# Kernel optimization log

Hardware: AMD Instinct MI355X
Metric: run time of the kernel (lower is better)

## Reference

```python
import jax, jax.numpy as jnp
import numpy as np

E, IN, H, OUT = 8, 512, 1024, 512   # num_experts, input_size, hidden_size, output_size
HH = H // 2                          # expert-MLP hidden (512)
GIN, GH = 5, E                       # gating GRU input / hidden


def gru_layer(x, w_ih, w_hh, b_ih, b_hh):
    """torch.nn.GRU single layer, batch_first. x: [B,T,I] -> ys: [B,T,Hd].
    Gate order in 3*Hd dims: reset, update, new."""
    Hd = w_hh.shape[1]
    def step(h, xt):
        gi = xt @ w_ih.T + b_ih          # [B,3Hd]
        gh = h @ w_hh.T + b_hh
        ir, iz, inn = jnp.split(gi, 3, axis=-1)
        hr, hz, hn = jnp.split(gh, 3, axis=-1)
        r = jax.nn.sigmoid(ir + hr)
        z = jax.nn.sigmoid(iz + hz)
        n = jnp.tanh(inn + r * hn)
        h = (1.0 - z) * n + z * h
        return h, h
    h0 = jnp.zeros((x.shape[0], Hd), x.dtype)
    _, ys = jax.lax.scan(step, h0, jnp.swapaxes(x, 0, 1))
    return jnp.swapaxes(ys, 0, 1)


def _uniform(key, shape, fan_in, fan_out):
    bound = np.sqrt(6.0 / (fan_in * fan_out))
    return jax.random.uniform(key, shape, jnp.float32, -bound, bound)


def setup_inputs() -> dict:
    key = jax.random.key(0)
    ks = jax.random.split(key, 16)
    g = 1.0 / np.sqrt(GH)
    m = 1.0 / np.sqrt(H)
    inp = {
        "X": jax.random.normal(ks[0], (128, 100, IN), jnp.float32),
        # gating GRU: 2 layers, input 5 -> hidden E
        "gw_ih0": jax.random.uniform(ks[1], (3 * GH, GIN), jnp.float32, -g, g),
        "gw_hh0": jax.random.uniform(ks[2], (3 * GH, GH), jnp.float32, -g, g),
        "gb_ih0": jnp.zeros((3 * GH,), jnp.float32),
        "gb_hh0": jnp.zeros((3 * GH,), jnp.float32),
        "gw_ih1": jax.random.uniform(ks[3], (3 * GH, GH), jnp.float32, -g, g),
        "gw_hh1": jax.random.uniform(ks[4], (3 * GH, GH), jnp.float32, -g, g),
        "gb_ih1": jnp.zeros((3 * GH,), jnp.float32),
        "gb_hh1": jnp.zeros((3 * GH,), jnp.float32),
        # main GRU: 1 layer, input IN -> hidden H
        "mw_ih": jax.random.uniform(ks[5], (3 * H, IN), jnp.float32, -m, m),
        "mw_hh": jax.random.uniform(ks[6], (3 * H, H), jnp.float32, -m, m),
        "mb_ih": jnp.zeros((3 * H,), jnp.float32),
        "mb_hh": jnp.zeros((3 * H,), jnp.float32),
        # expert MLP weights [E, in, out], biases [E, out]
        "w1": _uniform(ks[7], (E, H, HH), H, HH),
        "b1": jnp.zeros((E, HH), jnp.float32),
        "w2": _uniform(ks[8], (E, HH, HH), HH, HH),
        "b2": jnp.zeros((E, HH), jnp.float32),
        "w3": _uniform(ks[9], (E, HH, OUT), HH, OUT),
        "b3": jnp.zeros((E, OUT), jnp.float32),
    }
    return inp


def _moe_layer(x, coef, w, b):
    # same math as sum(x[...,None] * sum_e(coef_e * W_e), dim=1) + coef @ b
    return jnp.einsum("be,bi,eio->bo", coef, x, w) + coef @ b


def reference(X, gw_ih0, gw_hh0, gb_ih0, gb_hh0, gw_ih1, gw_hh1, gb_ih1, gb_hh1,
              mw_ih, mw_hh, mb_ih, mb_hh, w1, b1, w2, b2, w3, b3):
    Xg = X[:, :, -GIN:]
    h0 = gru_layer(Xg, gw_ih0, gw_hh0, gb_ih0, gb_hh0)
    h1 = gru_layer(h0, gw_ih1, gw_hh1, gb_ih1, gb_hh1)
    omega = jax.nn.softmax(h1[:, -1, :], axis=-1)          # [B,E]
    Z = gru_layer(X, mw_ih, mw_hh, mb_ih, mb_hh)[:, -1, :]  # [B,H]
    a1 = jax.nn.elu(_moe_layer(Z, omega, w1, b1))
    a2 = jax.nn.elu(_moe_layer(a1, omega, w2, b2))
    Y = _moe_layer(a2, omega, w3, b3)
    return jnp.clip(Y, 0.0, 1.0)
```

## Files before the change

### kernel.cpp

```cpp
#include <hip/hip_runtime.h>
#include <cmath>

#define B_   128
#define T_   100
#define IN_  512
#define H_   1024
#define E_   8
#define HH_  512
#define GIN_ 5
#define GH_  8

#define ALO_   0
#define BOFF_  81920
#define DUMP_  114688
#define HL_    81920
#define LDSZ5  147456
#define A_LOF 49152
#define BB_HI 98304
#define BB_LO 114688
#define LDSZF 131072

typedef unsigned long long u64t;
typedef unsigned int uint32;
typedef __attribute__((ext_vector_type(8)))  short bf16x8;
typedef __attribute__((ext_vector_type(4)))  float f32x4;
typedef __attribute__((ext_vector_type(16))) float f32x16;

__device__ __forceinline__ float sigf(float x) { return 1.0f / (1.0f + expf(-x)); }

__device__ __forceinline__ float4 ld_h4_sc1(const float4* p) {
  const u64t* q = (const u64t*)p;
  u64t a = __hip_atomic_load(q,     __ATOMIC_RELAXED, __HIP_MEMORY_SCOPE_AGENT);
  u64t b = __hip_atomic_load(q + 1, __ATOMIC_RELAXED, __HIP_MEMORY_SCOPE_AGENT);
  union { u64t u; float2 f; } ca, cb;
  ca.u = a; cb.u = b;
  return make_float4(ca.f.x, ca.f.y, cb.f.x, cb.f.y);
}

__device__ __forceinline__ void st_u64_sc1(void* p, u64t v) {
  __hip_atomic_store((u64t*)p, v, __ATOMIC_RELAXED, __HIP_MEMORY_SCOPE_AGENT);
}

__device__ __forceinline__ void gridbar(unsigned* c) {
  __syncthreads();
  if (threadIdx.x == 0) {
    __hip_atomic_fetch_add(c, 1u, __ATOMIC_RELEASE, __HIP_MEMORY_SCOPE_AGENT);
    while (__hip_atomic_load(c, __ATOMIC_RELAXED, __HIP_MEMORY_SCOPE_AGENT) < gridDim.x) {
      __builtin_amdgcn_s_sleep(1);
    }
  }
  __syncthreads();
}

__device__ __forceinline__ uint32 bf16_rne(float f) {
  uint32 u = __builtin_bit_cast(uint32, f);
  return (u + 0x7FFFu + ((u >> 16) & 1u)) >> 16;
}

__device__ __forceinline__ void split2(float f0, float f1, uint32& h, uint32& l) {
  uint32 h0 = bf16_rne(f0), h1 = bf16_rne(f1);
  float hf0 = __builtin_bit_cast(float, h0 << 16);
  float hf1 = __builtin_bit_cast(float, h1 << 16);
  uint32 l0 = bf16_rne(f0 - hf0), l1 = bf16_rne(f1 - hf1);
  h = h0 | (h1 << 16);
  l = l0 | (l1 << 16);
}

__device__ __forceinline__ void gl_lds16(const char* g, char* l) {
  __builtin_amdgcn_global_load_lds(
      (const __attribute__((address_space(1))) uint32*)(const void*)g,
      (__attribute__((address_space(3))) uint32*)(void*)l, 16, 0, 0);
}

__global__ __launch_bounds__(256) void xsplit_kernel(
    const float* __restrict__ X, char* __restrict__ xpl)
{
  int idx  = blockIdx.x * 256 + threadIdx.x;
  int lane = idx & 63;
  int bq   = (idx >> 6) & 3;
  int KT   = (idx >> 8) & 31;
  int t    = idx >> 13;
  int col  = lane & 31, kg = lane >> 5;
  int b    = bq * 32 + col;
  int k    = KT * 16 + kg * 8;
  const float* src = X + ((size_t)b * T_ + t) * IN_ + k;
  float4 va = *(const float4*)src;
  float4 vb = *(const float4*)(src + 4);
  uint32 h0,h1,h2,h3,l0,l1,l2,l3;
  split2(va.x, va.y, h0, l0); split2(va.z, va.w, h1, l1);
  split2(vb.x, vb.y, h2, l2); split2(vb.z, vb.w, h3, l3);
  size_t off = ((((size_t)t * 32 + KT) * 4 + bq) << 10) + ((size_t)lane << 4);
  *(uint4*)(xpl + off)            = make_uint4(h0, h1, h2, h3);
  *(uint4*)(xpl + 13107200 + off) = make_uint4(l0, l1, l2, l3);
}

__device__ __forceinline__ void stageS(
    char* lds, const char* xpl, const char* ringp,
    int t, int pn, int ko, int nt, int bq, int lane)
{
  const int KT = 8 * pn + ko;
  char* dst = lds + BOFF_ + ((pn & 1) << 15) + (ko << 12) + (nt << 11);
  const char *s0, *s1;
  if (KT < 32) {
    size_t o = ((((size_t)t * 32 + KT) * 4 + bq) << 10) + ((size_t)lane << 4);
    s0 = xpl + o;
    s1 = xpl + 13107200 + o;
  } else {
    size_t o = (size_t)t * 524288 + ((((size_t)(KT - 32) * 4) + bq) << 10) + ((size_t)lane << 4);
    s0 = ringp + o;
    s1 = ringp + 262144 + o;
  }
  gl_lds16(s0, dst);
  gl_lds16(s1, dst + 1024);
}

__global__ __launch_bounds__(1024, 4) void gru_mfma5(
    const char* __restrict__ xpl, char* __restrict__ ringp,
    const float* __restrict__ wih, const float* __restrict__ whh,
    const float* __restrict__ bih, const float* __restrict__ bhh,
    float* __restrict__ hq, unsigned* __restrict__ barr)
{
  extern __shared__ char lds[];
  const int tid  = threadIdx.x;
  const int lane = tid & 63;
  const int wv   = __builtin_amdgcn_readfirstlane(tid >> 6);
  const int q    = wv >> 1;
  const int ntc  = wv & 1;
  const int bid  = blockIdx.x;
  const int j0   = (bid >> 1) << 3;
  const int bhalf = bid & 1;
  const int bq   = bhalf * 2 + ntc;

  bf16x8 rah[12], ral2[2];
  {
    const int rrow = lane & 31, g = rrow >> 3, jl_a = rrow & 7, kg_a = lane >> 5;
    const int jA = j0 + jl_a;
    #pragma unroll
    for (int p = 0; p < 12; ++p) {
      const int KT = 8 * p + q;
      const int kb = KT * 16 + kg_a * 8;
      bf16x8 hi8, lo8;
      bool zero = (p <= 3) ? (g == 3) : (g == 2);
      if (zero) {
        #pragma unroll
        for (int e = 0; e < 8; ++e) { hi8[e] = 0; lo8[e] = 0; }
      } else {
        const float* srcp;
        if (p <= 3) srcp = wih + (size_t)(g * H_ + jA) * IN_ + kb;
        else        srcp = whh + (size_t)(((g == 3) ? 2 : g) * H_ + jA) * H_ + (kb - IN_);
        float4 va = *(const float4*)srcp;
        float4 vb = *(const float4*)(srcp + 4);
        float vv[8] = {va.x, va.y, va.z, va.w, vb.x, vb.y, vb.z, vb.w};
        #pragma unroll
        for (int e = 0; e < 8; ++e) {
          uint32 hb = bf16_rne(vv[e]);
          float hf = __builtin_bit_cast(float, hb << 16);
          uint32 lb = bf16_rne(vv[e] - hf);
          hi8[e] = (short)hb; lo8[e] = (short)lb;
        }
      }
      rah[p] = hi8;
      if (p <= 9) {
        if (ntc == 0)
          *(bf16x8*)(lds + ALO_ + (KT << 10) + (lane << 4)) = lo8;
      } else {
        ral2[p - 10] = lo8;
      }
    }
  }

  const int ejl = tid >> 6, eb = tid & 63;
  float bir = 0.f, biz = 0.f, bin = 0.f, bhr = 0.f, bhz = 0.f, bhn = 0.f;
  if (tid < 512) {
    int j = j0 + ejl;
    bir = bih[j]; biz = bih[H_ + j]; bin = bih[2 * H_ + j];
    bhr = bhh[j]; bhz = bhh[H_ + j]; bhn = bhh[2 * H_ + j];
  }
  float hprev_r = 0.f;
  __syncthreads();

  for (int t = 0; t < T_; ++t) {
    f32x16 acc = {0.f,0.f,0.f,0.f,0.f,0.f,0.f,0.f,0.f,0.f,0.f,0.f,0.f,0.f,0.f,0.f};

    stageS(lds, xpl, ringp, t, 0, q, ntc, bq, lane);

    #pragma unroll
    for (int p = 0; p < 12; ++p) {
      if (p < 11) {
        stageS(lds, xpl, ringp, t, p + 1, q, ntc, bq, lane);
        asm volatile("s_waitcnt vmcnt(2)" ::: "memory");
      } else {
        asm volatile("s_waitcnt vmcnt(0)" ::: "memory");
      }
      __builtin_amdgcn_s_barrier();
      __builtin_amdgcn_sched_barrier(0);
      {
        const int KT = 8 * p + q;
        bf16x8 al;
        if (p < 10) al = *(const bf16x8*)(lds + ALO_ + (KT << 10) + (lane << 4));
        else        al = ral2[p - 10];
        const char* bbp = lds + BOFF_ + ((p & 1) << 15) + (q << 12) + (ntc << 11);
        bf16x8 bh = *(const bf16x8*)(bbp + (lane << 4));
        bf16x8 bl = *(const bf16x8*)(bbp + 1024 + (lane << 4));
        acc = __builtin_amdgcn_mfma_f32_32x32x16_bf16(rah[p], bh, acc, 0, 0, 0);
        acc = __builtin_amdgcn_mfma_f32_32x32x16_bf16(rah[p], bl, acc, 0, 0, 0);
        acc = __builtin_amdgcn_mfma_f32_32x32x16_bf16(al,     bh, acc, 0, 0, 0);
      }
      __builtin_amdgcn_sched_barrier(0);
      __builtin_amdgcn_s_barrier();
    }

    float sv[4] = {0.f, 0.f, 0.f, 0.f};
    const int bb5 = eb >> 5, bl_ = eb & 31, jlh = ejl >> 2, jli = ejl & 3;
    const int laneoff = ((bl_ + (jlh << 5)) << 4) + (jli << 2);

    if (q < 4) {
      char* d = lds + DUMP_ + ((q & 3) << 13) + (ntc << 12) + (lane << 4);
      *(f32x4*)(d)          = (f32x4){acc[0],  acc[1],  acc[2],  acc[3]};
      *(f32x4*)(d + 1024)   = (f32x4){acc[4],  acc[5],  acc[6],  acc[7]};
      *(f32x4*)(d + 2048)   = (f32x4){acc[8],  acc[9],  acc[10], acc[11]};
      *(f32x4*)(d + 3072)   = (f32x4){acc[12], acc[13], acc[14], acc[15]};
    }
    __syncthreads();
    if (tid < 512) {
      #pragma unroll
      for (int qq = 0; qq < 4; ++qq) {
        const char* base = lds + DUMP_ + (qq << 13) + (bb5 << 12);
        #pragma unroll
        for (int g = 0; g < 4; ++g) sv[g] += *(const float*)(base + (g << 10) + laneoff);
      }
    }
    __syncthreads();
    if (q >= 4) {
      char* d = lds + DUMP_ + ((q & 3) << 13) + (ntc << 12) + (lane << 4);
      *(f32x4*)(d)          = (f32x4){acc[0],  acc[1],  acc[2],  acc[3]};
      *(f32x4*)(d + 1024)   = (f32x4){acc[4],  acc[5],  acc[6],  acc[7]};
      *(f32x4*)(d + 2048)   = (f32x4){acc[8],  acc[9],  acc[10], acc[11]};
      *(f32x4*)(d + 3072)   = (f32x4){acc[12], acc[13], acc[14], acc[15]};
    }
    __syncthreads();
    if (tid < 512) {
      #pragma unroll
      for (int qq = 0; qq < 4; ++qq) {
        const char* base = lds + DUMP_ + (qq << 13) + (bb5 << 12);
        #pragma unroll
        for (int g = 0; g < 4; ++g) sv[g] += *(const float*)(base + (g << 10) + laneoff);
      }
      float rr = sigf(sv[0] + bir + bhr);
      float zz = sigf(sv[1] + biz + bhz);
      float nn = tanhf(sv[2] + bin + rr * (sv[3] + bhn));
      float hv = (1.f - zz) * nn + zz * hprev_r;
      hprev_r = hv;
      ((float*)(lds + HL_))[(ejl << 6) + eb] = hv;
      if (t == T_ - 1) hq[(size_t)(bhalf * 64 + eb) * H_ + (j0 + ejl)] = hv;
    }
    __syncthreads();

    if (tid < 64) {
      const int b = tid;
      const float* hl = (const float*)(lds + HL_);
      uint32 hi16[8], lo16[8];
      #pragma unroll
      for (int jl = 0; jl < 8; ++jl) {
        float v = hl[(jl << 6) + b];
        uint32 hb = bf16_rne(v);
        float hf = __builtin_bit_cast(float, hb << 16);
        lo16[jl] = bf16_rne(v - hf);
        hi16[jl] = hb;
      }
      u64t H0 = (u64t)hi16[0] | ((u64t)hi16[1] << 16) | ((u64t)hi16[2] << 32) | ((u64t)hi16[3] << 48);
      u64t H1 = (u64t)hi16[4] | ((u64t)hi16[5] << 16) | ((u64t)hi16[6] << 32) | ((u64t)hi16[7] << 48);
      u64t L0 = (u64t)lo16[0] | ((u64t)lo16[1] << 16) | ((u64t)lo16[2] << 32) | ((u64t)lo16[3] << 48);
      u64t L1 = (u64t)lo16[4] | ((u64t)lo16[5] << 16) | ((u64t)lo16[6] << 32) | ((u64t)lo16[7] << 48);
      const int kg  = (bid >> 1) & 1;
      const int KTh = bid >> 2;
      const int bq2 = bhalf * 2 + (b >> 5);
      const int lane_f = (b & 31) + (kg << 5);
      size_t off = ((((size_t)KTh << 2) + bq2) << 10) + ((size_t)lane_f << 4);
      char* basep = ringp + (size_t)(t + 1) * 524288;
      st_u64_sc1(basep + off, H0);
      st_u64_sc1(basep + off + 8, H1);
      st_u64_sc1(basep + 262144 + off, L0);
      st_u64_sc1(basep + 262144 + off + 8, L1);
    }
    gridbar(barr + t);
  }
}

__device__ __forceinline__ int boff(int kt, int nt, int lane) {
  return (((((kt << 3) + nt) << 6) + lane) << 4) ^ ((nt & 3) << 5);
}

__global__ __launch_bounds__(256) void xt_kernel(
    const float* __restrict__ X, float4* __restrict__ XT4)
{
  int idx = blockIdx.x * 256 + threadIdx.x;
  int b  = idx & 127;
  int kq = (idx >> 7) & 127;
  int t  = idx >> 14;
  XT4[idx] = *(const float4*)(X + ((size_t)b * T_ + t) * IN_ + kq * 4);
}

template<bool RING>
__global__ __launch_bounds__(1024, 4) void gru_mfma(
    const float4* __restrict__ XT4, const float* __restrict__ X, int use_xt,
    const float* __restrict__ wih, const float* __restrict__ whh,
    const float* __restrict__ bih, const float* __restrict__ bhh,
    float* __restrict__ ring, unsigned* __restrict__ barr)
{
  extern __shared__ char lds[];
  const int tid  = threadIdx.x;
  const int lane = tid & 63;
  const int wv   = __builtin_amdgcn_readfirstlane(tid >> 6);
  const int nt   = wv & 7;
  const int ktw  = wv >> 3;
  const int j0   = blockIdx.x << 2;

  for (int ii = tid * 2; ii < 24576; ii += 2048) {
    int r = ii / 1536, k = ii - r * 1536;
    int jj = r & 3, g = r >> 2;
    float f0, f1;
    if (k < IN_) {
      if (g == 3) { f0 = 0.f; f1 = 0.f; }
      else {
        const float* p = wih + (size_t)(((g == 2 ? 2 : g) * H_) + j0 + jj) * IN_ + k;
        f0 = p[0]; f1 = p[1];
      }
    } else {
      if (g == 2) { f0 = 0.f; f1 = 0.f; }
      else {
        const float* p = whh + (size_t)(((g == 3 ? 2 : g) * H_) + j0 + jj) * H_ + (k - IN_);
        f0 = p[0]; f1 = p[1];
      }
    }
    uint32 h, l; split2(f0, f1, h, l);
    int KT = k >> 5, k32 = k & 31;
    int ln  = r + ((k32 >> 3) << 4);
    int off = (KT << 10) + (ln << 4) + ((k32 & 7) << 1);
    *(uint32*)(lds + off)         = h;
    *(uint32*)(lds + A_LOF + off) = l;
  }

  const int ejj = tid >> 7, eb = tid & 127;
  float bir = 0.f, biz = 0.f, bin = 0.f, bhr = 0.f, bhz = 0.f, bhn = 0.f;
  if (tid < 512) {
    int j = j0 + ejj;
    bir = bih[j]; biz = bih[H_ + j]; bin = bih[2 * H_ + j];
    bhr = bhh[j]; bhz = bhh[H_ + j]; bhn = bhh[2 * H_ + j];
  }
  __syncthreads();

  const int kq_loc = tid >> 7;
  const int sb     = tid & 127;
  const int s_nt   = sb >> 4;
  const int lane_w = (sb & 15) + ((kq_loc >> 1) << 4);
  const int sub8   = (kq_loc & 1) << 3;

  for (int t = 0; t < T_; ++t) {
    const float4* __restrict__ hp4 =
        (const float4*)ring + (size_t)(RING ? t : (t & 1)) * 32768;
    float* __restrict__ hnf =
        ring + (size_t)(RING ? (t + 1) : ((t + 1) & 1)) * 131072;
    const float4* __restrict__ xt_t = XT4 + (size_t)t * 16384;

    f32x4 acc = {0.f, 0.f, 0.f, 0.f};

    #pragma unroll 1
    for (int c = 0; c < 24; ++c) {
      #pragma unroll
      for (int i = 0; i < 2; ++i) {
        int kqg = (c << 4) + kq_loc + (i << 3);
        float4 v;
        if (kqg < 128) {
          if (use_xt) v = xt_t[kqg * 128 + sb];
          else        v = *(const float4*)(X + ((size_t)sb * T_ + t) * IN_ + (kqg << 2));
        } else {
          v = RING ? hp4[(kqg - 128) * 128 + sb]
                   : ld_h4_sc1(hp4 + (kqg - 128) * 128 + sb);
        }
        uint32 h01, h23, l01, l23;
        split2(v.x, v.y, h01, l01);
        split2(v.z, v.w, h23, l23);
        int bo = boff(i, s_nt, lane_w) + sub8;
        *(uint2*)(lds + BB_HI + bo) = make_uint2(h01, h23);
        *(uint2*)(lds + BB_LO + bo) = make_uint2(l01, l23);
      }
      __syncthreads();
      {
        int KT = (c << 1) + ktw;
        bf16x8 ah = *(const bf16x8*)(lds + (KT << 10) + (lane << 4));
        bf16x8 al = *(const bf16x8*)(lds + A_LOF + (KT << 10) + (lane << 4));
        int bo = boff(ktw, nt, lane);
        bf16x8 bh = *(const bf16x8*)(lds + BB_HI + bo);
        bf16x8 bl = *(const bf16x8*)(lds + BB_LO + bo);
        acc = __builtin_amdgcn_mfma_f32_16x16x32_bf16(ah, bh, acc, 0, 0, 0);
        acc = __builtin_amdgcn_mfma_f32_16x16x32_bf16(ah, bl, acc, 0, 0, 0);
        acc = __builtin_amdgcn_mfma_f32_16x16x32_bf16(al, bh, acc, 0, 0, 0);
      }
      __syncthreads();
    }

    *(f32x4*)(lds + BB_HI + boff(ktw, nt, lane)) = acc;
    __syncthreads();
    if (tid < 512) {
      float sv[4];
      #pragma unroll
      for (int g = 0; g < 4; ++g) {
        int r  = (g << 2) + ejj;
        int lr = (eb & 15) + ((r >> 2) << 4);
        int rg = (r & 3) << 2;
        float v0 = *(const float*)(lds + BB_HI + boff(0, eb >> 4, lr) + rg);
        float v1 = *(const float*)(lds + BB_HI + boff(1, eb >> 4, lr) + rg);
        sv[g] = v0 + v1;
      }
      float rr = sigf(sv[0] + bir + bhr);
      float zz = sigf(sv[1] + biz + bhz);
      float nn = tanhf(sv[2] + bin + rr * (sv[3] + bhn));
      int hidx = ((blockIdx.x * 128 + eb) << 2) + ejj;
      float hpv;
      if (RING) hpv = ((const float*)hp4)[hidx];
      else      hpv = __hip_atomic_load(&((const float*)hp4)[hidx],
                                        __ATOMIC_RELAXED, __HIP_MEMORY_SCOPE_AGENT);
      float hv = (1.f - zz) * nn + zz * hpv;
      __hip_atomic_store(&hnf[hidx], hv, __ATOMIC_RELAXED, __HIP_MEMORY_SCOPE_AGENT);
    }
    gridbar(barr + t);
  }
}

__global__ __launch_bounds__(256) void hfin_kernel(
    const float* __restrict__ h4, float* __restrict__ out)
{
  int idx = blockIdx.x * 256 + threadIdx.x;
  int b = idx >> 10, k = idx & 1023;
  out[idx] = h4[(((k >> 2) * 128 + b) << 2) + (k & 3)];
}

__global__ __launch_bounds__(64, 1) void gating_kernel(
    const float* __restrict__ X,
    const float* __restrict__ gwih0, const float* __restrict__ gwhh0,
    const float* __restrict__ gbih0, const float* __restrict__ gbhh0,
    const float* __restrict__ gwih1, const float* __restrict__ gwhh1,
    const float* __restrict__ gbih1, const float* __restrict__ gbhh1,
    float* __restrict__ omega)
{
  const int b = blockIdx.x;
  const int g = threadIdx.x;
  const int u = g & 7;
  float wi0[GIN_] = {}, wh0[GH_] = {}, wi1[GH_] = {}, wh1[GH_] = {};
  float bi0 = 0.f, bh0 = 0.f, bi1 = 0.f, bh1 = 0.f;
  if (g < 3 * GH_) {
    #pragma unroll
    for (int i = 0; i < GIN_; ++i) wi0[i] = gwih0[g * GIN_ + i];
    #pragma unroll
    for (int k = 0; k < GH_; ++k) { wh0[k] = gwhh0[g * GH_ + k]; wi1[k] = gwih1[g * GH_ + k]; wh1[k] = gwhh1[g * GH_ + k]; }
    bi0 = gbih0[g]; bh0 = gbhh0[g]; bi1 = gbih1[g]; bh1 = gbhh1[g];
  }
  float h0[GH_] = {}, h1[GH_] = {};
  for (int t = 0; t < T_; ++t) {
    float xt[GIN_];
    #pragma unroll
    for (int i = 0; i < GIN_; ++i) xt[i] = X[((size_t)b * T_ + t) * IN_ + (IN_ - GIN_) + i];
    float px = bi0, ph = bh0;
    #pragma unroll
    for (int i = 0; i < GIN_; ++i) px = fmaf(xt[i], wi0[i], px);
    #pragma unroll
    for (int k = 0; k < GH_; ++k) ph = fmaf(h0[k], wh0[k], ph);
    float s = px + ph;
    float s_r = __shfl(s, u);
    float s_z = __shfl(s, 8 + u);
    float nval = tanhf(px + sigf(s_r) * ph);
    float zval = sigf(s_z);
    float hnew = (1.f - zval) * nval + zval * h0[u];
    #pragma unroll
    for (int k = 0; k < GH_; ++k) h0[k] = __shfl(hnew, 16 + k);
    float px1 = bi1, ph1 = bh1;
    #pragma unroll
    for (int k = 0; k < GH_; ++k) px1 = fmaf(h0[k], wi1[k], px1);
    #pragma unroll
    for (int k = 0; k < GH_; ++k) ph1 = fmaf(h1[k], wh1[k], ph1);
    float s1 = px1 + ph1;
    float s1r = __shfl(s1, u);
    float s1z = __shfl(s1, 8 + u);
    float n1 = tanhf(px1 + sigf(s1r) * ph1);
    float z1 = sigf(s1z);
    float h1new = (1.f - z1) * n1 + z1 * h1[u];
    #pragma unroll
    for (int k = 0; k < GH_; ++k) h1[k] = __shfl(h1new, 16 + k);
  }
  if (g < GH_) {
    float m = h1[0];
    #pragma unroll
    for (int k = 1; k < GH_; ++k) m = fmaxf(m, h1[k]);
    float sum = 0.f;
    #pragma unroll
    for (int k = 0; k < GH_; ++k) sum += expf(h1[k] - m);
    omega[b * GH_ + g] = expf(h1[g] - m) / sum;
  }
}

__global__ __launch_bounds__(256, 2) void moe_kernel(
    const float* __restrict__ in, const float* __restrict__ w,
    const float* __restrict__ bias, const float* __restrict__ omega,
    float* __restrict__ out, int K, int act)
{
  __shared__ float4 lin4[64 * 32];
  __shared__ float  ldsw[E_ * 4 * 128];
  const int tid  = threadIdx.x;
  const int bh   = blockIdx.x & 1;
  const int jt   = blockIdx.x >> 1;
  const int wv   = tid >> 6;
  const int lane = tid & 63;
  const int j0   = jt * 4;
  const int j    = __builtin_amdgcn_readfirstlane(j0 + wv);
  const int b    = bh * 64 + lane;

  float acc[E_] = {0.f,0.f,0.f,0.f,0.f,0.f,0.f,0.f};
  const float4* row4 = &lin4[lane * 32];
  const int nch = K / 128;

  for (int c = 0; c < nch; ++c) {
    __syncthreads();
    const int k0 = c * 128;
    #pragma unroll
    for (int it = 0; it < 8; ++it) {
      int f = it * 256 + tid;
      int bb = f >> 5, qq = f & 31;
      float4 v = *(const float4*)(in + (size_t)(bh * 64 + bb) * K + k0 + qq * 4);
      lin4[bb * 32 + ((qq & 24) | ((qq ^ bb) & 7))] = v;
    }
    #pragma unroll
    for (int it = 0; it < 4; ++it) {
      int f = it * 256 + tid;
      int e = f >> 7, k = f & 127;
      float4 v = *(const float4*)(w + ((size_t)e * K + k0 + k) * HH_ + j0);
      ldsw[(e * 4 + 0) * 128 + k] = v.x;
      ldsw[(e * 4 + 1) * 128 + k] = v.y;
      ldsw[(e * 4 + 2) * 128 + k] = v.z;
      ldsw[(e * 4 + 3) * 128 + k] = v.w;
    }
    __syncthreads();
    #pragma unroll 2
    for (int qq = 0; qq < 32; ++qq) {
      float4 xv = row4[(qq & 24) | ((qq ^ lane) & 7)];
      #pragma unroll
      for (int e = 0; e < E_; ++e) {
        const float4 wq = *(const float4*)&ldsw[(e * 4 + wv) * 128 + 4 * qq];
        acc[e] = fmaf(xv.x, wq.x, acc[e]);
        acc[e] = fmaf(xv.y, wq.y, acc[e]);
        acc[e] = fmaf(xv.z, wq.z, acc[e]);
        acc[e] = fmaf(xv.w, wq.w, acc[e]);
      }
    }
  }

  float om[E_];
  #pragma unroll
  for (int e = 0; e < E_; ++e) om[e] = omega[b * E_ + e];
  float v = 0.f;
  #pragma unroll
  for (int e = 0; e < E_; ++e) v = fmaf(om[e], acc[e] + bias[e * HH_ + j], v);
  if (act == 0) v = (v > 0.f) ? v : expm1f(v);
  else          v = fminf(fmaxf(v, 0.f), 1.f);
  out[(size_t)b * HH_ + j] = v;
}

extern "C" void kernel_launch(void* const* d_in, const int* in_sizes, int n_in,
                              void* d_out, int out_size, void* d_ws, size_t ws_size,
                              hipStream_t stream) {
  (void)in_sizes; (void)n_in; (void)out_size;
  const float* X     = (const float*)d_in[0];
  const float* gwih0 = (const float*)d_in[1];
  const float* gwhh0 = (const float*)d_in[2];
  const float* gbih0 = (const float*)d_in[3];
  const float* gbhh0 = (const float*)d_in[4];
  const float* gwih1 = (const float*)d_in[5];
  const float* gwhh1 = (const float*)d_in[6];
  const float* gbih1 = (const float*)d_in[7];
  const float* gbhh1 = (const float*)d_in[8];
  const float* mwih  = (const float*)d_in[9];
  const float* mwhh  = (const float*)d_in[10];
  const float* mbih  = (const float*)d_in[11];
  const float* mbhh  = (const float*)d_in[12];
  const float* w1    = (const float*)d_in[13];
  const float* b1    = (const float*)d_in[14];
  const float* w2    = (const float*)d_in[15];
  const float* b2    = (const float*)d_in[16];
  const float* w3    = (const float*)d_in[17];
  const float* b3    = (const float*)d_in[18];

  const size_t HBUF = (size_t)B_ * H_;
  size_t tierS_f = 256 + HBUF + 101 * HBUF + 1024 + 2 * (size_t)B_ * HH_ + HBUF + 6553600;
  const size_t XTF = (size_t)T_ * IN_ * B_;
  size_t ringA = 256 + (size_t)(T_ + 1) * HBUF + HBUF + 1024 + 2 * (size_t)B_ * HH_ + XTF;
  size_t ringB = 256 + 2 * HBUF + HBUF + 1024 + 2 * (size_t)B_ * HH_ + XTF;

  float* ws = (float*)d_ws;

  if (ws_size >= tierS_f * sizeof(float)) {
    unsigned* barr = (unsigned*)ws;
    float* hq    = ws + 256;
    float* ringp = hq + HBUF;
    float* om    = ringp + 101 * HBUF;
    float* a1    = om + 1024;
    float* a2    = a1 + (size_t)B_ * HH_;
    float* xpl   = a2 + (size_t)B_ * HH_ + HBUF;

    (void)hipMemsetAsync(d_ws, 0, 256 * sizeof(float), stream);
    (void)hipMemsetAsync(ringp, 0, 524288, stream);
    (void)hipFuncSetAttribute((const void*)gru_mfma5,
                        hipFuncAttributeMaxDynamicSharedMemorySize, LDSZ5);

    gating_kernel<<<128, 64, 0, stream>>>(X, gwih0, gwhh0, gbih0, gbhh0,
                                          gwih1, gwhh1, gbih1, gbhh1, om);
    xsplit_kernel<<<3200, 256, 0, stream>>>(X, (char*)xpl);
    gru_mfma5<<<256, 1024, LDSZ5, stream>>>((const char*)xpl, (char*)ringp,
        mwih, mwhh, mbih, mbhh, hq, barr);
    moe_kernel<<<256, 256, 0, stream>>>(hq, w1, b1, om, a1, H_, 0);
    moe_kernel<<<256, 256, 0, stream>>>(a1, w2, b2, om, a2, HH_, 0);
    moe_kernel<<<256, 256, 0, stream>>>(a2, w3, b3, om, (float*)d_out, HH_, 1);
    return;
  }

  int tierA   = ws_size >= ringA * sizeof(float);
  int use_xt  = tierA || (ws_size >= ringB * sizeof(float));
  int R       = tierA ? (T_ + 1) : 2;

  unsigned* barr = (unsigned*)ws;
  float* ring = ws + 256;
  float* hfin = ring + (size_t)R * HBUF;
  float* om   = hfin + HBUF;
  float* a1   = om + 1024;
  float* a2   = a1 + (size_t)B_ * HH_;
  float* XT   = a2 + (size_t)B_ * HH_;

  (void)hipMemsetAsync(d_ws, 0, (256 + HBUF) * sizeof(float), stream);
  (void)hipFuncSetAttribute((const void*)gru_mfma<true>,
                      hipFuncAttributeMaxDynamicSharedMemorySize, LDSZF);
  (void)hipFuncSetAttribute((const void*)gru_mfma<false>,
                      hipFuncAttributeMaxDynamicSharedMemorySize, LDSZF);

  gating_kernel<<<128, 64, 0, stream>>>(X, gwih0, gwhh0, gbih0, gbhh0,
                                        gwih1, gwhh1, gbih1, gbhh1, om);
  if (use_xt)
    xt_kernel<<<(T_ * 128 * 128) / 256, 256, 0, stream>>>(X, (float4*)XT);

  if (tierA)
    gru_mfma<true><<<256, 1024, LDSZF, stream>>>((const float4*)XT, X, use_xt,
        mwih, mwhh, mbih, mbhh, ring, barr);
  else
    gru_mfma<false><<<256, 1024, LDSZF, stream>>>((const float4*)XT, X, use_xt,
        mwih, mwhh, mbih, mbhh, ring, barr);

  const float* hlast = ring + (size_t)(tierA ? T_ : (T_ & 1)) * HBUF;
  hfin_kernel<<<512, 256, 0, stream>>>(hlast, hfin);
  moe_kernel<<<256, 256, 0, stream>>>(hfin, w1, b1, om, a1, H_, 0);
  moe_kernel<<<256, 256, 0, stream>>>(a1, w2, b2, om, a2, HH_, 0);
  moe_kernel<<<256, 256, 0, stream>>>(a2, w3, b3, om, (float*)d_out, HH_, 1);
}
```

Baseline: 1.537 ms.

## Hoist next-step input-projection phases before grid barrier and slim the gate epilogue

The persistent GRU kernel now computes the first four K-phases of the next timestep, which depend only on X, before waiting on the grid barrier. This overlaps input-projection MFMA work with the cross-block synchronisation latency. The epilogue also drops the two-pass accumulator dump: all eight wave accumulators are written into the B staging area at once, reduced with vector loads by 128 threads each handling 4 hidden units, then packed into bf16 hi/lo and stored to the ring directly. This removes several __syncthreads and the separate HL_ pack pass, in exchange for more complex phase bookkeeping and reuse of the staging LDS region.

```diff
diff --git a/kernel.cpp b/kernel.cpp
--- a/kernel.cpp
+++ b/kernel.cpp
@@ -12,8 +12,6 @@
 
 #define ALO_   0
 #define BOFF_  81920
-#define DUMP_  114688
-#define HL_    81920
 #define LDSZ5  147456
 #define A_LOF 49152
 #define BB_HI 98304
@@ -114,7 +112,28 @@
   gl_lds16(s1, dst + 1024);
 }
 
-__global__ __launch_bounds__(1024, 4) void gru_mfma5(
+__device__ __forceinline__ void phase_mfma(
+    const char* lds, int p, int q, int ntc, int lane,
+    const bf16x8* rah, const bf16x8* ral2, f32x16& acc)
+{
+  const int KT = 8 * p + q;
+  bf16x8 al;
+  if (p < 10) al = *(const bf16x8*)(lds + ALO_ + (KT << 10) + (lane << 4));
+  else        al = ral2[p - 10];
+  const char* bbp = lds + BOFF_ + ((p & 1) << 15) + (q << 12) + (ntc << 11);
+  bf16x8 bh = *(const bf16x8*)(bbp + (lane << 4));
+  bf16x8 bl = *(const bf16x8*)(bbp + 1024 + (lane << 4));
+  acc = __builtin_amdgcn_mfma_f32_32x32x16_bf16(rah[p], bh, acc, 0, 0, 0);
+  acc = __builtin_amdgcn_mfma_f32_32x32x16_bf16(rah[p], bl, acc, 0, 0, 0);
+  acc = __builtin_amdgcn_mfma_f32_32x32x16_bf16(al,     bh, acc, 0, 0, 0);
+}
+
+#define VMCNT2 asm volatile("s_waitcnt vmcnt(2)" ::: "memory")
+#define VMCNT0 asm volatile("s_waitcnt vmcnt(0)" ::: "memory")
+#define SBAR   __builtin_amdgcn_s_barrier()
+#define SCHB   __builtin_amdgcn_sched_barrier(0)
+
+__global__ __launch_bounds__(1024, 4) void gru_mfma6(
     const char* __restrict__ xpl, char* __restrict__ ringp,
     const float* __restrict__ wih, const float* __restrict__ whh,
     const float* __restrict__ bih, const float* __restrict__ bhh,
@@ -169,121 +188,112 @@
     }
   }
 
-  const int ejl = tid >> 6, eb = tid & 63;
-  float bir = 0.f, biz = 0.f, bin = 0.f, bhr = 0.f, bhz = 0.f, bhn = 0.f;
-  if (tid < 512) {
-    int j = j0 + ejl;
-    bir = bih[j]; biz = bih[H_ + j]; bin = bih[2 * H_ + j];
-    bhr = bhh[j]; bhz = bhh[H_ + j]; bhn = bhh[2 * H_ + j];
-  }
-  float hprev_r = 0.f;
+  const int eb  = tid & 63;
+  const int ehi = (tid >> 6) & 1;
+  f32x4 bir4 = {0,0,0,0}, biz4 = {0,0,0,0}, bin4 = {0,0,0,0};
+  f32x4 bhr4 = {0,0,0,0}, bhz4 = {0,0,0,0}, bhn4 = {0,0,0,0};
+  if (tid < 128) {
+    const int jb = j0 + ehi * 4;
+    bir4 = *(const f32x4*)&bih[jb];
+    biz4 = *(const f32x4*)&bih[H_ + jb];
+    bin4 = *(const f32x4*)&bih[2 * H_ + jb];
+    bhr4 = *(const f32x4*)&bhh[jb];
+    bhz4 = *(const f32x4*)&bhh[H_ + jb];
+    bhn4 = *(const f32x4*)&bhh[2 * H_ + jb];
+  }
+  float hp4[4] = {0.f, 0.f, 0.f, 0.f};
   __syncthreads();
 
+  f32x16 acc = {0.f,0.f,0.f,0.f,0.f,0.f,0.f,0.f,0.f,0.f,0.f,0.f,0.f,0.f,0.f,0.f};
+
+  stageS(lds, xpl, ringp, 0, 0, q, ntc, bq, lane);
+  stageS(lds, xpl, ringp, 0, 1, q, ntc, bq, lane);
+  VMCNT2; SBAR; SCHB; phase_mfma(lds, 0, q, ntc, lane, rah, ral2, acc); SCHB; SBAR;
+  stageS(lds, xpl, ringp, 0, 2, q, ntc, bq, lane);
+  VMCNT2; SBAR; SCHB; phase_mfma(lds, 1, q, ntc, lane, rah, ral2, acc); SCHB; SBAR;
+  stageS(lds, xpl, ringp, 0, 3, q, ntc, bq, lane);
+  VMCNT2; SBAR; SCHB; phase_mfma(lds, 2, q, ntc, lane, rah, ral2, acc); SCHB; SBAR;
+  VMCNT0; SBAR; SCHB; phase_mfma(lds, 3, q, ntc, lane, rah, ral2, acc); SCHB; SBAR;
+
   for (int t = 0; t < T_; ++t) {
-    f32x16 acc = {0.f,0.f,0.f,0.f,0.f,0.f,0.f,0.f,0.f,0.f,0.f,0.f,0.f,0.f,0.f,0.f};
-
-    stageS(lds, xpl, ringp, t, 0, q, ntc, bq, lane);
-
-    #pragma unroll
-    for (int p = 0; p < 12; ++p) {
-      if (p < 11) {
-        stageS(lds, xpl, ringp, t, p + 1, q, ntc, bq, lane);
-        asm volatile("s_waitcnt vmcnt(2)" ::: "memory");
-      } else {
-        asm volatile("s_waitcnt vmcnt(0)" ::: "memory");
-      }
-      __builtin_amdgcn_s_barrier();
-      __builtin_amdgcn_sched_barrier(0);
-      {
-        const int KT = 8 * p + q;
-        bf16x8 al;
-        if (p < 10) al = *(const bf16x8*)(lds + ALO_ + (KT << 10) + (lane << 4));
-        else        al = ral2[p - 10];
-        const char* bbp = lds + BOFF_ + ((p & 1) << 15) + (q << 12) + (ntc << 11);
-        bf16x8 bh = *(const bf16x8*)(bbp + (lane << 4));
-        bf16x8 bl = *(const bf16x8*)(bbp + 1024 + (lane << 4));
-        acc = __builtin_amdgcn_mfma_f32_32x32x16_bf16(rah[p], bh, acc, 0, 0, 0);
-        acc = __builtin_amdgcn_mfma_f32_32x32x16_bf16(rah[p], bl, acc, 0, 0, 0);
-        acc = __builtin_amdgcn_mfma_f32_32x32x16_bf16(al,     bh, acc, 0, 0, 0);
-      }
-      __builtin_amdgcn_sched_barrier(0);
-      __builtin_amdgcn_s_barrier();
-    }
-
-    float sv[4] = {0.f, 0.f, 0.f, 0.f};
-    const int bb5 = eb >> 5, bl_ = eb & 31, jlh = ejl >> 2, jli = ejl & 3;
-    const int laneoff = ((bl_ + (jlh << 5)) << 4) + (jli << 2);
-
-    if (q < 4) {
-      char* d = lds + DUMP_ + ((q & 3) << 13) + (ntc << 12) + (lane << 4);
-      *(f32x4*)(d)          = (f32x4){acc[0],  acc[1],  acc[2],  acc[3]};
-      *(f32x4*)(d + 1024)   = (f32x4){acc[4],  acc[5],  acc[6],  acc[7]};
-      *(f32x4*)(d + 2048)   = (f32x4){acc[8],  acc[9],  acc[10], acc[11]};
-      *(f32x4*)(d + 3072)   = (f32x4){acc[12], acc[13], acc[14], acc[15]};
+    stageS(lds, xpl, ringp, t, 4, q, ntc, bq, lane);
+    #pragma unroll
+    for (int p = 4; p <= 10; ++p) {
+      stageS(lds, xpl, ringp, t, p + 1, q, ntc, bq, lane);
+      VMCNT2; SBAR; SCHB;
+      phase_mfma(lds, p, q, ntc, lane, rah, ral2, acc);
+      SCHB; SBAR;
+    }
+    VMCNT0; SBAR; SCHB;
+    phase_mfma(lds, 11, q, ntc, lane, rah, ral2, acc);
+    SCHB; SBAR;
+
+    {
+      char* d = lds + BOFF_ + (q << 13) + (ntc << 12) + (lane << 4);
+      *(f32x4*)(d)        = (f32x4){acc[0],  acc[1],  acc[2],  acc[3]};
+      *(f32x4*)(d + 1024) = (f32x4){acc[4],  acc[5],  acc[6],  acc[7]};
+      *(f32x4*)(d + 2048) = (f32x4){acc[8],  acc[9],  acc[10], acc[11]};
+      *(f32x4*)(d + 3072) = (f32x4){acc[12], acc[13], acc[14], acc[15]};
     }
     __syncthreads();
-    if (tid < 512) {
+
+    if (tid < 128) {
+      const int lane_w = (eb & 31) + (ehi << 5);
+      const int bb5 = eb >> 5;
+      f32x4 s0 = {0,0,0,0}, s1 = {0,0,0,0}, s2 = {0,0,0,0}, s3 = {0,0,0,0};
       #pragma unroll
-      for (int qq = 0; qq < 4; ++qq) {
-        const char* base = lds + DUMP_ + (qq << 13) + (bb5 << 12);
-        #pragma unroll
-        for (int g = 0; g < 4; ++g) sv[g] += *(const float*)(base + (g << 10) + laneoff);
-      }
-    }
-    __syncthreads();
-    if (q >= 4) {
-      char* d = lds + DUMP_ + ((q & 3) << 13) + (ntc << 12) + (lane << 4);
-      *(f32x4*)(d)          = (f32x4){acc[0],  acc[1],  acc[2],  acc[3]};
-      *(f32x4*)(d + 1024)   = (f32x4){acc[4],  acc[5],  acc[6],  acc[7]};
-      *(f32x4*)(d + 2048)   = (f32x4){acc[8],  acc[9],  acc[10], acc[11]};
-      *(f32x4*)(d + 3072)   = (f32x4){acc[12], acc[13], acc[14], acc[15]};
-    }
-    __syncthreads();
-    if (tid < 512) {
+      for (int qq = 0; qq < 8; ++qq) {
+        const char* base = lds + BOFF_ + (qq << 13) + (bb5 << 12) + (lane_w << 4);
+        s0 += *(const f32x4*)(base);
+        s1 += *(const f32x4*)(base + 1024);
+        s2 += *(const f32x4*)(base + 2048);
+        s3 += *(const f32x4*)(base + 3072);
+      }
+      uint32 hh[4], ll[4];
+      float hv4[4];
       #pragma unroll
-      for (int qq = 0; qq < 4; ++qq) {
-        const char* base = lds + DUMP_ + (qq << 13) + (bb5 << 12);
-        #pragma unroll
-        for (int g = 0; g < 4; ++g) sv[g] += *(const float*)(base + (g << 10) + laneoff);
-      }
-      float rr = sigf(sv[0] + bir + bhr);
-      float zz = sigf(sv[1] + biz + bhz);
-      float nn = tanhf(sv[2] + bin + rr * (sv[3] + bhn));
-      float hv = (1.f - zz) * nn + zz * hprev_r;
-      hprev_r = hv;
-      ((float*)(lds + HL_))[(ejl << 6) + eb] = hv;
-      if (t == T_ - 1) hq[(size_t)(bhalf * 64 + eb) * H_ + (j0 + ejl)] = hv;
-    }
-    __syncthreads();
-
-    if (tid < 64) {
-      const int b = tid;
-      const float* hl = (const float*)(lds + HL_);
-      uint32 hi16[8], lo16[8];
-      #pragma unroll
-      for (int jl = 0; jl < 8; ++jl) {
-        float v = hl[(jl << 6) + b];
-        uint32 hb = bf16_rne(v);
+      for (int jli = 0; jli < 4; ++jli) {
+        float rr = sigf(s0[jli] + bir4[jli] + bhr4[jli]);
+        float zz = sigf(s1[jli] + biz4[jli] + bhz4[jli]);
+        float nn = tanhf(s2[jli] + bin4[jli] + rr * (s3[jli] + bhn4[jli]));
+        float hv = (1.f - zz) * nn + zz * hp4[jli];
+        hp4[jli] = hv; hv4[jli] = hv;
+        uint32 hb = bf16_rne(hv);
         float hf = __builtin_bit_cast(float, hb << 16);
-        lo16[jl] = bf16_rne(v - hf);
-        hi16[jl] = hb;
-      }
-      u64t H0 = (u64t)hi16[0] | ((u64t)hi16[1] << 16) | ((u64t)hi16[2] << 32) | ((u64t)hi16[3] << 48);
-      u64t H1 = (u64t)hi16[4] | ((u64t)hi16[5] << 16) | ((u64t)hi16[6] << 32) | ((u64t)hi16[7] << 48);
-      u64t L0 = (u64t)lo16[0] | ((u64t)lo16[1] << 16) | ((u64t)lo16[2] << 32) | ((u64t)lo16[3] << 48);
-      u64t L1 = (u64t)lo16[4] | ((u64t)lo16[5] << 16) | ((u64t)lo16[6] << 32) | ((u64t)lo16[7] << 48);
+        ll[jli] = bf16_rne(hv - hf);
+        hh[jli] = hb;
+      }
+      u64t HI = (u64t)hh[0] | ((u64t)hh[1] << 16) | ((u64t)hh[2] << 32) | ((u64t)hh[3] << 48);
+      u64t LO = (u64t)ll[0] | ((u64t)ll[1] << 16) | ((u64t)ll[2] << 32) | ((u64t)ll[3] << 48);
       const int kg  = (bid >> 1) & 1;
       const int KTh = bid >> 2;
-      const int bq2 = bhalf * 2 + (b >> 5);
-      const int lane_f = (b & 31) + (kg << 5);
-      size_t off = ((((size_t)KTh << 2) + bq2) << 10) + ((size_t)lane_f << 4);
+      const int bq2 = bhalf * 2 + (eb >> 5);
+      const int lane_f = (eb & 31) + (kg << 5);
+      size_t off = ((((size_t)KTh << 2) + bq2) << 10) + ((size_t)lane_f << 4) + ((size_t)ehi << 3);
       char* basep = ringp + (size_t)(t + 1) * 524288;
-      st_u64_sc1(basep + off, H0);
-      st_u64_sc1(basep + off + 8, H1);
-      st_u64_sc1(basep + 262144 + off, L0);
-      st_u64_sc1(basep + 262144 + off + 8, L1);
-    }
-    gridbar(barr + t);
+      st_u64_sc1(basep + off, HI);
+      st_u64_sc1(basep + 262144 + off, LO);
+      if (t == T_ - 1)
+        *(float4*)&hq[(size_t)(bhalf * 64 + eb) * H_ + j0 + 4 * ehi] =
+            make_float4(hv4[0], hv4[1], hv4[2], hv4[3]);
+    }
+
+    if (t < T_ - 1) {
+      asm volatile("s_waitcnt lgkmcnt(0)" ::: "memory");
+      SCHB; SBAR;
+
+      acc = (f32x16){0.f,0.f,0.f,0.f,0.f,0.f,0.f,0.f,0.f,0.f,0.f,0.f,0.f,0.f,0.f,0.f};
+      stageS(lds, xpl, ringp, t + 1, 0, q, ntc, bq, lane);
+      stageS(lds, xpl, ringp, t + 1, 1, q, ntc, bq, lane);
+      VMCNT2; SBAR; SCHB; phase_mfma(lds, 0, q, ntc, lane, rah, ral2, acc); SCHB; SBAR;
+      stageS(lds, xpl, ringp, t + 1, 2, q, ntc, bq, lane);
+      VMCNT2; SBAR; SCHB; phase_mfma(lds, 1, q, ntc, lane, rah, ral2, acc); SCHB; SBAR;
+      stageS(lds, xpl, ringp, t + 1, 3, q, ntc, bq, lane);
+      VMCNT2; SBAR; SCHB; phase_mfma(lds, 2, q, ntc, lane, rah, ral2, acc); SCHB; SBAR;
+      VMCNT0; SBAR; SCHB; phase_mfma(lds, 3, q, ntc, lane, rah, ral2, acc); SCHB; SBAR;
+
+      gridbar(barr + t);
+    }
   }
 }
 
@@ -608,13 +618,13 @@
 
     (void)hipMemsetAsync(d_ws, 0, 256 * sizeof(float), stream);
     (void)hipMemsetAsync(ringp, 0, 524288, stream);
-    (void)hipFuncSetAttribute((const void*)gru_mfma5,
+    (void)hipFuncSetAttribute((const void*)gru_mfma6,
                         hipFuncAttributeMaxDynamicSharedMemorySize, LDSZ5);
 
     gating_kernel<<<128, 64, 0, stream>>>(X, gwih0, gwhh0, gbih0, gbhh0,
                                           gwih1, gwhh1, gbih1, gbhh1, om);
     xsplit_kernel<<<3200, 256, 0, stream>>>(X, (char*)xpl);
-    gru_mfma5<<<256, 1024, LDSZ5, stream>>>((const char*)xpl, (char*)ringp,
+    gru_mfma6<<<256, 1024, LDSZ5, stream>>>((const char*)xpl, (char*)ringp,
         mwih, mwhh, mbih, mbhh, hq, barr);
     moe_kernel<<<256, 256, 0, stream>>>(hq, w1, b1, om, a1, H_, 0);
     moe_kernel<<<256, 256, 0, stream>>>(a1, w2, b2, om, a2, HH_, 0);
```

After: 2.889 ms. 1.88x slower.
